# Kernel tuning notes

Hardware: AMD Instinct MI355X
Metric: run time of the kernel (lower is better)

Reference implementation:

```python
import jax, jax.numpy as jnp
import numpy as np


def setup_inputs() -> dict:
    key = jax.random.key(0)
    k1, k2, k3 = jax.random.split(key, 3)
    B, H, S, D = 2, 8, 4096, 64
    queries = jax.random.normal(k1, (B, H, S, D), dtype=jnp.float32)
    keys = jax.random.normal(k2, (B, H, S, D), dtype=jnp.float32)
    values = jax.random.normal(k3, (B, H, S, D), dtype=jnp.float32)
    mask = jnp.zeros((1, 1, S, S), dtype=jnp.float32)
    return {"queries": queries, "keys": keys, "values": values, "d_k": D, "mask": mask}


def reference(queries, keys, values, d_k, mask):
    # scores: [B, H, Sq, Sk]
    scale = 1.0 / jnp.sqrt(jnp.asarray(d_k, dtype=queries.dtype))
    scores = jnp.einsum("bhqd,bhkd->bhqk", queries, keys) * scale
    scores = scores + (-1e9) * mask  # additive mask, broadcasts over B, H
    weights = jax.nn.softmax(scores, axis=-1)
    return jnp.einsum("bhqk,bhkd->bhqd", weights, values)
```

## Files before the change

### kernel.cpp

```cpp
#include <hip/hip_runtime.h>

#define S_LEN 4096
#define DHEAD 64
#define BK    64
#define NT    (S_LEN / BK)
#define TILE_HALFS (BK * DHEAD)

typedef __fp16   pk16x2 __attribute__((ext_vector_type(2)));
typedef _Float16 half8  __attribute__((ext_vector_type(8)));
typedef float    f32x16 __attribute__((ext_vector_type(16)));
typedef unsigned uint2v __attribute__((ext_vector_type(2)));

#define MFMA32(a, b, c) __builtin_amdgcn_mfma_f32_32x32x16_f16(a, b, c, 0, 0, 0)

__device__ __forceinline__ unsigned pk2u(float a, float b) {
    union { pk16x2 p; unsigned u; } x;
    x.p = __builtin_amdgcn_cvt_pkrtz(a, b);
    return x.u;
}

__device__ __forceinline__ uint2v pls(unsigned x, unsigned y) {
    return __builtin_amdgcn_permlane32_swap(x, y, false, false);
}
__device__ __forceinline__ float xmax32(float v) {
    uint2v r = pls(__float_as_uint(v), __float_as_uint(v));
    return fmaxf(__uint_as_float(r.x), __uint_as_float(r.y));
}
__device__ __forceinline__ float xadd32(float v) {
    uint2v r = pls(__float_as_uint(v), __float_as_uint(v));
    return __uint_as_float(r.x) + __uint_as_float(r.y);
}

__global__ void mask_flag_kernel(const float4* __restrict__ mask, int* __restrict__ flag) {
    const long stride = 2048L * 256;
    long i = (long)blockIdx.x * 256 + threadIdx.x;
    int nz = 0;
    #pragma unroll
    for (int it = 0; it < 8; ++it) {
        float4 a = mask[i + it * stride];
        nz |= (a.x != 0.f) | (a.y != 0.f) | (a.z != 0.f) | (a.w != 0.f);
    }
    if (__any(nz)) {
        if ((threadIdx.x & 63) == 0) atomicOr(flag, 1);
    }
}

__global__ __launch_bounds__(256, 2) void attn32p_kernel(
    const float* __restrict__ Q, const float* __restrict__ K,
    const float* __restrict__ V, const int* __restrict__ dkp,
    const float* __restrict__ mask, const int* __restrict__ maskflag,
    float* __restrict__ O)
{
    const int bid = blockIdx.x;
    const int L   = (bid & 7) * 64 + (bid >> 3);
    const int bh  = L >> 5;
    const int qt  = L & 31;

    const int tid  = threadIdx.x;
    const int w    = tid >> 6;
    const int lane = tid & 63;
    const int l31  = lane & 31;
    const int h    = lane >> 5;
    const int cx   = lane & 7;
    const int vkey = (l31 ^ (l31 >> 3)) & 7;

    const long gbase = (long)bh * S_LEN * DHEAD;
    const float* Qh = Q + gbase;
    const float* Kh = K + gbase;
    const float* Vh = V + gbase;

    const int q0 = qt * 128 + w * 32;
    const float csq  = rsqrtf((float)dkp[0]) * 1.44269504088896f;
    const float mfac = -1e9f * 1.44269504088896f;
    const bool use_mask = (maskflag[0] != 0);

    __shared__ __align__(16) _Float16 KT[4][TILE_HALFS];
    __shared__ __align__(16) _Float16 VT[4][TILE_HALFS];

    half8 qf[4];
    #pragma unroll
    for (int ks = 0; ks < 4; ++ks) {
        const float4* src = (const float4*)(Qh + (long)(q0 + l31) * DHEAD + ks * 16 + h * 8);
        float4 a = src[0], b = src[1];
        union { unsigned u[4]; half8 h8; } u;
        u.u[0] = pk2u(a.x * csq, a.y * csq);
        u.u[1] = pk2u(a.z * csq, a.w * csq);
        u.u[2] = pk2u(b.x * csq, b.y * csq);
        u.u[3] = pk2u(b.z * csq, b.w * csq);
        qf[ks] = u.h8;
    }

    const int kr  = tid >> 2;
    const int ks4 = tid & 3;
    const int vrp = tid >> 3;
    const int vdq = tid & 7;
    const float* Kb = Kh + (long)kr * DHEAD + ks4 * 16;
    const float* Vb = Vh + (long)(2 * vrp) * DHEAD + vdq * 8;
    const int kcol0 = (((2 * ks4)     ^ (kr & 7)) << 3);
    const int kcol1 = (((2 * ks4 + 1) ^ (kr & 7)) << 3);
    const int vd0   = vdq * 8;
    const int voct  = vrp >> 2;
    const int vlow  = (2 * vrp) & 7;

    float4 kf[4], vf[4];
    auto load_tile = [&](int kt) {
        const float4* kp  = (const float4*)(Kb + (long)kt * TILE_HALFS);
        kf[0] = kp[0]; kf[1] = kp[1]; kf[2] = kp[2]; kf[3] = kp[3];
        const float4* vp0 = (const float4*)(Vb + (long)kt * TILE_HALFS);
        const float4* vp1 = (const float4*)(Vb + (long)kt * TILE_HALFS + DHEAD);
        vf[0] = vp0[0]; vf[1] = vp0[1]; vf[2] = vp1[0]; vf[3] = vp1[1];
    };
    auto store_tile = [&](int bb) {
        union { unsigned u[4]; half8 h8; } u0, u1;
        u0.u[0] = pk2u(kf[0].x, kf[0].y);
        u0.u[1] = pk2u(kf[0].z, kf[0].w);
        u0.u[2] = pk2u(kf[1].x, kf[1].y);
        u0.u[3] = pk2u(kf[1].z, kf[1].w);
        u1.u[0] = pk2u(kf[2].x, kf[2].y);
        u1.u[1] = pk2u(kf[2].z, kf[2].w);
        u1.u[2] = pk2u(kf[3].x, kf[3].y);
        u1.u[3] = pk2u(kf[3].z, kf[3].w);
        *(half8*)&KT[bb][kr * 64 + kcol0] = u0.h8;
        *(half8*)&KT[bb][kr * 64 + kcol1] = u1.h8;
        _Float16* vt = &VT[bb][0];
        #define VCOL(j) ((((voct ^ (j) ^ vdq) & 7) << 3) + vlow)
        *(pk16x2*)&vt[(vd0 + 0) * 64 + VCOL(0)] = __builtin_amdgcn_cvt_pkrtz(vf[0].x, vf[2].x);
        *(pk16x2*)&vt[(vd0 + 1) * 64 + VCOL(1)] = __builtin_amdgcn_cvt_pkrtz(vf[0].y, vf[2].y);
        *(pk16x2*)&vt[(vd0 + 2) * 64 + VCOL(2)] = __builtin_amdgcn_cvt_pkrtz(vf[0].z, vf[2].z);
        *(pk16x2*)&vt[(vd0 + 3) * 64 + VCOL(3)] = __builtin_amdgcn_cvt_pkrtz(vf[0].w, vf[2].w);
        *(pk16x2*)&vt[(vd0 + 4) * 64 + VCOL(4)] = __builtin_amdgcn_cvt_pkrtz(vf[1].x, vf[3].x);
        *(pk16x2*)&vt[(vd0 + 5) * 64 + VCOL(5)] = __builtin_amdgcn_cvt_pkrtz(vf[1].y, vf[3].y);
        *(pk16x2*)&vt[(vd0 + 6) * 64 + VCOL(6)] = __builtin_amdgcn_cvt_pkrtz(vf[1].z, vf[3].z);
        *(pk16x2*)&vt[(vd0 + 7) * 64 + VCOL(7)] = __builtin_amdgcn_cvt_pkrtz(vf[1].w, vf[3].w);
        #undef VCOL
    };

    auto qk = [&](int bb, f32x16& sa, f32x16& sb) {
        __builtin_amdgcn_s_setprio(1);
        #pragma unroll
        for (int ks = 0; ks < 4; ++ks) {
            const int off = (((2 * ks + h) ^ cx) << 3);
            half8 a0 = *(const half8*)&KT[bb][(l31 << 6) + off];
            half8 a1 = *(const half8*)&KT[bb][2048 + (l31 << 6) + off];
            sa = MFMA32(a0, qf[ks], sa);
            sb = MFMA32(a1, qf[ks], sb);
        }
        __builtin_amdgcn_s_setprio(0);
    };

    f32x16 o0 = {0.f,0.f,0.f,0.f,0.f,0.f,0.f,0.f,0.f,0.f,0.f,0.f,0.f,0.f,0.f,0.f};
    f32x16 o1 = o0;
    float m_i = -INFINITY;
    float l_i = 0.0f;

    auto pv = [&](int bb, const f32x16& sa, const f32x16& sb) {
        unsigned wp[16];
        #pragma unroll
        for (int d = 0; d < 8; ++d) {
            wp[d]     = pk2u(sa[2*d], sa[2*d+1]);
            wp[8 + d] = pk2u(sb[2*d], sb[2*d+1]);
        }
        __builtin_amdgcn_s_setprio(1);
        #pragma unroll
        for (int si = 0; si < 4; ++si) {
            const int bs = (si >> 1) * 8 + (si & 1) * 4;
            uint2v r0 = pls(wp[bs + 0], wp[bs + 2]);
            uint2v r1 = pls(wp[bs + 1], wp[bs + 3]);
            union { unsigned u[4]; half8 h8; } pa;
            pa.u[0] = r0.x; pa.u[1] = r1.x; pa.u[2] = r0.y; pa.u[3] = r1.y;
            const int voff = (((2 * si + h) ^ vkey) << 3);
            half8 v0 = *(const half8*)&VT[bb][(l31 << 6) + voff];
            half8 v1 = *(const half8*)&VT[bb][2048 + (l31 << 6) + (voff ^ 32)];
            o0 = MFMA32(pa.h8, v0, o0);
            o1 = MFMA32(pa.h8, v1, o1);
        }
        __builtin_amdgcn_s_setprio(0);
    };

    load_tile(0); store_tile(0);
    load_tile(1); store_tile(1);
    __syncthreads();

    for (int kt = 0; kt < NT; kt += 2) {
        const int b0 = kt & 3, b1 = (kt + 1) & 3;

        if (kt + 2 < NT) load_tile(kt + 2);

        f32x16 s0 = {0.f,0.f,0.f,0.f,0.f,0.f,0.f,0.f,0.f,0.f,0.f,0.f,0.f,0.f,0.f,0.f};
        f32x16 s1 = s0, s2 = s0, s3 = s0;
        qk(b0, s0, s1);
        if (kt + 2 < NT) store_tile((kt + 2) & 3);

        if (kt + 3 < NT) load_tile(kt + 3);
        qk(b1, s2, s3);

        if (use_mask) {
            const float* mrow = mask + (long)(q0 + l31) * S_LEN + kt * BK;
            #pragma unroll
            for (int r = 0; r < 16; ++r) {
                const int k = (r & 3) + ((r >> 2) << 3) + (h << 2);
                s0[r] += mfac * mrow[k];
                s1[r] += mfac * mrow[32 + k];
                s2[r] += mfac * mrow[BK + k];
                s3[r] += mfac * mrow[BK + 32 + k];
            }
        }

        {
            float tt[16];
            #pragma unroll
            for (int i = 0; i < 8; ++i) {
                tt[i]     = fmaxf(fmaxf(s0[2*i], s0[2*i+1]), fmaxf(s1[2*i], s1[2*i+1]));
                tt[8 + i] = fmaxf(fmaxf(s2[2*i], s2[2*i+1]), fmaxf(s3[2*i], s3[2*i+1]));
            }
            #pragma unroll
            for (int i = 0; i < 8; ++i) tt[i] = fmaxf(tt[i], tt[8 + i]);
            float mx = fmaxf(fmaxf(fmaxf(tt[0], tt[1]), fmaxf(tt[2], tt[3])),
                             fmaxf(fmaxf(tt[4], tt[5]), fmaxf(tt[6], tt[7])));
            mx = xmax32(mx);
            const bool need = __any(mx > m_i + 8.0f);
            const float mnew = need ? fmaxf(m_i, mx) : m_i;
            float ra = 0.f, rb = 0.f;
            #pragma unroll
            for (int r = 0; r < 16; ++r) {
                float p0 = __builtin_amdgcn_exp2f(s0[r] - mnew);
                float p1 = __builtin_amdgcn_exp2f(s1[r] - mnew);
                float p2 = __builtin_amdgcn_exp2f(s2[r] - mnew);
                float p3 = __builtin_amdgcn_exp2f(s3[r] - mnew);
                s0[r] = p0; s1[r] = p1; s2[r] = p2; s3[r] = p3;
                ra += p0 + p1; rb += p2 + p3;
            }
            float rsum = xadd32(ra + rb);
            if (need) {
                const float alpha = __builtin_amdgcn_exp2f(m_i - mnew);
                #pragma unroll
                for (int r = 0; r < 16; ++r) {
                    const int qr = (r & 3) + ((r >> 2) << 3) + (h << 2);
                    float a_r = __shfl(alpha, qr, 64);
                    o0[r] *= a_r; o1[r] *= a_r;
                }
                l_i = alpha * l_i + rsum;
                m_i = mnew;
            } else {
                l_i += rsum;
            }
        }

        if (kt + 3 < NT) store_tile((kt + 3) & 3);

        pv(b0, s0, s1);
        pv(b1, s2, s3);

        if (kt + 2 < NT) __syncthreads();
    }

    float* dst = O + gbase;
    #pragma unroll
    for (int r = 0; r < 16; ++r) {
        const int qr = (r & 3) + ((r >> 2) << 3) + (h << 2);
        float lq = __shfl(l_i, qr, 64);
        float inv = __builtin_amdgcn_rcpf(lq);
        const long row = (long)(q0 + qr) * DHEAD;
        dst[row + l31]      = o0[r] * inv;
        dst[row + 32 + l31] = o1[r] * inv;
    }
}

extern "C" void kernel_launch(void* const* d_in, const int* in_sizes, int n_in,
                              void* d_out, int out_size, void* d_ws, size_t ws_size,
                              hipStream_t stream) {
    const float* Q    = (const float*)d_in[0];
    const float* K    = (const float*)d_in[1];
    const float* V    = (const float*)d_in[2];
    const int*   dk   = (const int*)d_in[3];
    const float* mask = (const float*)d_in[4];
    float* out = (float*)d_out;
    int* flag = (int*)d_ws;

    (void)hipMemsetAsync(flag, 0, sizeof(int), stream);
    mask_flag_kernel<<<2048, 256, 0, stream>>>((const float4*)mask, flag);

    attn32p_kernel<<<512, 256, 0, stream>>>(Q, K, V, dk, mask, flag, out);
}
```

Measured before the change: 251.6 us.

## Process softmax and PV per key tile instead of per tile pair

```diff
diff --git a/kernel.cpp b/kernel.cpp
--- a/kernel.cpp
+++ b/kernel.cpp
@@ -45,7 +45,7 @@
     }
 }
 
-__global__ __launch_bounds__(256, 2) void attn32p_kernel(
+__global__ __launch_bounds__(256, 2) void attn32r_kernel(
     const float* __restrict__ Q, const float* __restrict__ K,
     const float* __restrict__ V, const int* __restrict__ dkp,
     const float* __restrict__ mask, const int* __restrict__ maskflag,
@@ -135,6 +135,11 @@
         #undef VCOL
     };
 
+    f32x16 o0 = {0.f,0.f,0.f,0.f,0.f,0.f,0.f,0.f,0.f,0.f,0.f,0.f,0.f,0.f,0.f,0.f};
+    f32x16 o1 = o0;
+    float m_i = -INFINITY;
+    float l_i = 0.0f;
+
     auto qk = [&](int bb, f32x16& sa, f32x16& sb) {
         __builtin_amdgcn_s_setprio(1);
         #pragma unroll
@@ -147,12 +152,48 @@
         }
         __builtin_amdgcn_s_setprio(0);
     };
-
-    f32x16 o0 = {0.f,0.f,0.f,0.f,0.f,0.f,0.f,0.f,0.f,0.f,0.f,0.f,0.f,0.f,0.f,0.f};
-    f32x16 o1 = o0;
-    float m_i = -INFINITY;
-    float l_i = 0.0f;
-
+    auto addmask = [&](int kt, f32x16& sa, f32x16& sb) {
+        const float* mrow = mask + (long)(q0 + l31) * S_LEN + kt * BK;
+        #pragma unroll
+        for (int r = 0; r < 16; ++r) {
+            const int k = (r & 3) + ((r >> 2) << 3) + (h << 2);
+            sa[r] += mfac * mrow[k];
+            sb[r] += mfac * mrow[32 + k];
+        }
+    };
+    auto softmax = [&](f32x16& sa, f32x16& sb) {
+        float tt[8];
+        #pragma unroll
+        for (int i = 0; i < 8; ++i)
+            tt[i] = fmaxf(fmaxf(sa[2*i], sa[2*i+1]), fmaxf(sb[2*i], sb[2*i+1]));
+        float mx = fmaxf(fmaxf(fmaxf(tt[0], tt[1]), fmaxf(tt[2], tt[3])),
+                         fmaxf(fmaxf(tt[4], tt[5]), fmaxf(tt[6], tt[7])));
+        mx = xmax32(mx);
+        const bool need = __any(mx > m_i + 8.0f);
+        const float mnew = need ? fmaxf(m_i, mx) : m_i;
+        float ra = 0.f, rb = 0.f;
+        #pragma unroll
+        for (int r = 0; r < 16; ++r) {
+            float p0 = __builtin_amdgcn_exp2f(sa[r] - mnew);
+            float p1 = __builtin_amdgcn_exp2f(sb[r] - mnew);
+            sa[r] = p0; sb[r] = p1;
+            ra += p0; rb += p1;
+        }
+        float rsum = xadd32(ra + rb);
+        if (need) {
+            const float alpha = __builtin_amdgcn_exp2f(m_i - mnew);
+            #pragma unroll
+            for (int r = 0; r < 16; ++r) {
+                const int qr = (r & 3) + ((r >> 2) << 3) + (h << 2);
+                float a_r = __shfl(alpha, qr, 64);
+                o0[r] *= a_r; o1[r] *= a_r;
+            }
+            l_i = alpha * l_i + rsum;
+            m_i = mnew;
+        } else {
+            l_i += rsum;
+        }
+    };
     auto pv = [&](int bb, const f32x16& sa, const f32x16& sb) {
         unsigned wp[16];
         #pragma unroll
@@ -185,70 +226,21 @@
         const int b0 = kt & 3, b1 = (kt + 1) & 3;
 
         if (kt + 2 < NT) load_tile(kt + 2);
-
         f32x16 s0 = {0.f,0.f,0.f,0.f,0.f,0.f,0.f,0.f,0.f,0.f,0.f,0.f,0.f,0.f,0.f,0.f};
-        f32x16 s1 = s0, s2 = s0, s3 = s0;
+        f32x16 s1 = s0;
         qk(b0, s0, s1);
         if (kt + 2 < NT) store_tile((kt + 2) & 3);
+        if (use_mask) addmask(kt, s0, s1);
+        softmax(s0, s1);
+        pv(b0, s0, s1);
 
         if (kt + 3 < NT) load_tile(kt + 3);
+        f32x16 s2 = {0.f,0.f,0.f,0.f,0.f,0.f,0.f,0.f,0.f,0.f,0.f,0.f,0.f,0.f,0.f,0.f};
+        f32x16 s3 = s2;
         qk(b1, s2, s3);
-
-        if (use_mask) {
-            const float* mrow = mask + (long)(q0 + l31) * S_LEN + kt * BK;
-            #pragma unroll
-            for (int r = 0; r < 16; ++r) {
-                const int k = (r & 3) + ((r >> 2) << 3) + (h << 2);
-                s0[r] += mfac * mrow[k];
-                s1[r] += mfac * mrow[32 + k];
-                s2[r] += mfac * mrow[BK + k];
-                s3[r] += mfac * mrow[BK + 32 + k];
-            }
-        }
-
-        {
-            float tt[16];
-            #pragma unroll
-            for (int i = 0; i < 8; ++i) {
-                tt[i]     = fmaxf(fmaxf(s0[2*i], s0[2*i+1]), fmaxf(s1[2*i], s1[2*i+1]));
-                tt[8 + i] = fmaxf(fmaxf(s2[2*i], s2[2*i+1]), fmaxf(s3[2*i], s3[2*i+1]));
-            }
-            #pragma unroll
-            for (int i = 0; i < 8; ++i) tt[i] = fmaxf(tt[i], tt[8 + i]);
-            float mx = fmaxf(fmaxf(fmaxf(tt[0], tt[1]), fmaxf(tt[2], tt[3])),
-                             fmaxf(fmaxf(tt[4], tt[5]), fmaxf(tt[6], tt[7])));
-            mx = xmax32(mx);
-            const bool need = __any(mx > m_i + 8.0f);
-            const float mnew = need ? fmaxf(m_i, mx) : m_i;
-            float ra = 0.f, rb = 0.f;
-            #pragma unroll
-            for (int r = 0; r < 16; ++r) {
-                float p0 = __builtin_amdgcn_exp2f(s0[r] - mnew);
-                float p1 = __builtin_amdgcn_exp2f(s1[r] - mnew);
-                float p2 = __builtin_amdgcn_exp2f(s2[r] - mnew);
-                float p3 = __builtin_amdgcn_exp2f(s3[r] - mnew);
-                s0[r] = p0; s1[r] = p1; s2[r] = p2; s3[r] = p3;
-                ra += p0 + p1; rb += p2 + p3;
-            }
-            float rsum = xadd32(ra + rb);
-            if (need) {
-                const float alpha = __builtin_amdgcn_exp2f(m_i - mnew);
-                #pragma unroll
-                for (int r = 0; r < 16; ++r) {
-                    const int qr = (r & 3) + ((r >> 2) << 3) + (h << 2);
-                    float a_r = __shfl(alpha, qr, 64);
-                    o0[r] *= a_r; o1[r] *= a_r;
-                }
-                l_i = alpha * l_i + rsum;
-                m_i = mnew;
-            } else {
-                l_i += rsum;
-            }
-        }
-
         if (kt + 3 < NT) store_tile((kt + 3) & 3);
-
-        pv(b0, s0, s1);
+        if (use_mask) addmask(kt + 1, s2, s3);
+        softmax(s2, s3);
         pv(b1, s2, s3);
 
         if (kt + 2 < NT) __syncthreads();
@@ -280,5 +272,5 @@
     (void)hipMemsetAsync(flag, 0, sizeof(int), stream);
     mask_flag_kernel<<<2048, 256, 0, stream>>>((const float4*)mask, flag);
 
-    attn32p_kernel<<<512, 256, 0, stream>>>(Q, K, V, dk, mask, flag, out);
-}
+    attn32r_kernel<<<512, 256, 0, stream>>>(Q, K, V, dk, mask, flag, out);
+}
```

Measured after the change: 246.8 us. Within noise of the previous version (-1.9%).
